# Kernel optimization log

Measured on AMD Instinct MI355X. Metric: run time of the kernel, lower is better.

## Reference

```python
import jax, jax.numpy as jnp
import numpy as np

VO, SO, VIN, SM = 16, 100, 16, 100
B, N, K = 2, 8192, 30
EPS = 1e-8

def _split(x, nv):
    v = x[..., :3 * nv].reshape(x.shape[:-1] + (nv, 3))
    s = x[..., 3 * nv:]
    return v, s

def _merge(v, s):
    return jnp.concatenate([v.reshape(v.shape[:-2] + (-1,)), s], axis=-1)

def _vnorm(v):  # [..., nv, 3] -> [..., nv]
    return jnp.sqrt(jnp.sum(v * v, axis=-1) + EPS)

def gvp(x, nv_in, Wh, Wv, Ws, bs, nls=True, nlv=True):
    v, s = _split(x, nv_in)
    vh = jnp.einsum('...ic,ih->...hc', v, Wh)          # vi -> h vector linear
    vn = _vnorm(vh)                                     # rotation-invariant norms
    s_out = jnp.concatenate([s, vn], axis=-1) @ Ws + bs
    if nls:
        s_out = jax.nn.relu(s_out)
    v_out = jnp.einsum('...hc,ho->...oc', vh, Wv)       # h -> vo vector linear
    if nlv:
        v_out = v_out * jax.nn.sigmoid(_vnorm(v_out))[..., None]
    return _merge(v_out, s_out)

def gvp_layernorm(x, nv, g, b):
    v, s = _split(x, nv)
    vn2 = jnp.sum(v * v, axis=-1, keepdims=True)        # [..., nv, 1]
    denom = jnp.sqrt(jnp.mean(vn2, axis=-2, keepdims=True) + EPS)
    v = v / denom
    mu = jnp.mean(s, axis=-1, keepdims=True)
    var = jnp.var(s, axis=-1, keepdims=True)
    s = (s - mu) / jnp.sqrt(var + 1e-5) * g + b
    return _merge(v, s)

def setup_inputs() -> dict:
    key = jax.random.key(0)
    ks = jax.random.split(key, 24)
    def W(i, shape):
        return jax.random.normal(ks[i], shape, dtype=jnp.float32) / np.float32(np.sqrt(shape[0]))
    d = {}
    d['h_V'] = jax.random.normal(ks[0], (B, N, 3 * VO + SO), dtype=jnp.float32)
    d['h_M'] = jax.random.normal(ks[1], (B, N, K, 3 * VIN + SM), dtype=jnp.float32)
    d['mask_V'] = jax.random.randint(ks[2], (B, N), 0, 2, dtype=jnp.int32)
    d['mask_attend'] = jax.random.randint(ks[3], (B, N, K), 0, 2, dtype=jnp.int32)
    # W_EV: GVP(vi=32,si=200,vo=16,so=100,h=32) -> GVP(16,100,16,100) -> GVP(16,100,16,100,no nl)
    d['Wh1'] = W(4, (32, 32)); d['Wv1'] = W(5, (32, 16)); d['Ws1'] = W(6, (232, 100)); d['bs1'] = jnp.zeros((100,), jnp.float32)
    d['Wh2'] = W(7, (16, 16)); d['Wv2'] = W(8, (16, 16)); d['Ws2'] = W(9, (116, 100)); d['bs2'] = jnp.zeros((100,), jnp.float32)
    d['Wh3'] = W(10, (16, 16)); d['Wv3'] = W(11, (16, 16)); d['Ws3'] = W(12, (116, 100)); d['bs3'] = jnp.zeros((100,), jnp.float32)
    # W_dh: GVP(vi=16,si=100,vo=32,so=400,h=32) -> GVP(vi=32,si=400,vo=16,so=100,h=32,no nl)
    d['Wh4'] = W(13, (16, 32)); d['Wv4'] = W(14, (32, 32)); d['Ws4'] = W(15, (132, 400)); d['bs4'] = jnp.zeros((400,), jnp.float32)
    d['Wh5'] = W(16, (32, 32)); d['Wv5'] = W(17, (32, 16)); d['Ws5'] = W(18, (432, 100)); d['bs5'] = jnp.zeros((100,), jnp.float32)
    d['ln0_g'] = jnp.ones((SO,), jnp.float32); d['ln0_b'] = jnp.zeros((SO,), jnp.float32)
    d['ln1_g'] = jnp.ones((SO,), jnp.float32); d['ln1_b'] = jnp.zeros((SO,), jnp.float32)
    return d

def reference(h_V, h_M, mask_V, mask_attend,
              Wh1, Wv1, Ws1, bs1, Wh2, Wv2, Ws2, bs2, Wh3, Wv3, Ws3, bs3,
              Wh4, Wv4, Ws4, bs4, Wh5, Wv5, Ws5, bs5,
              ln0_g, ln0_b, ln1_g, ln1_b):
    # expand node features over neighbor axis and vs_concat with messages
    hVe = jnp.broadcast_to(h_V[:, :, None, :], (B, N, K, h_V.shape[-1]))
    vV, sV = _split(hVe, VO)
    vM, sM = _split(h_M, VIN)
    h_EV = _merge(jnp.concatenate([vV, vM], axis=-2), jnp.concatenate([sV, sM], axis=-1))
    m = gvp(h_EV, VO + VIN, Wh1, Wv1, Ws1, bs1)
    m = gvp(m, VO, Wh2, Wv2, Ws2, bs2)
    m = gvp(m, VO, Wh3, Wv3, Ws3, bs3, nls=False, nlv=False)
    m = mask_attend[..., None].astype(jnp.float32) * m
    dh = jnp.mean(m, axis=2)
    h = gvp_layernorm(h_V + dh, VO, ln0_g, ln0_b)  # dropout rate 0 -> identity
    dh2 = gvp(h, VO, Wh4, Wv4, Ws4, bs4)
    dh2 = gvp(dh2, 2 * VO, Wh5, Wv5, Ws5, bs5, nls=False, nlv=False)
    h = gvp_layernorm(h + dh2, VO, ln1_g, ln1_b)
    h = mask_V[..., None].astype(jnp.float32) * h
    return h
```

## Files before the change

kernel.cpp:

```cpp
#include <hip/hip_runtime.h>

#define KK 30
#define F 148
#define NNODE 16384

typedef short bf16x8 __attribute__((ext_vector_type(8)));
typedef float f32x4v __attribute__((ext_vector_type(4)));

__device__ __forceinline__ ushort f2bf(float x) {
  unsigned u = __float_as_uint(x);
  unsigned r = (u + 0x7FFF + ((u >> 16) & 1)) >> 16;
  return (ushort)r;
}
__device__ __forceinline__ float bf2f(ushort b) { return __uint_as_float(((unsigned)b) << 16); }
__device__ __forceinline__ void bsplit(float x, ushort& h, ushort& l) {
  ushort hh = f2bf(x); h = hh; l = f2bf(x - bf2f(hh));
}

#define WS_S1B 0
#define WS_VHB (NNODE * 100)
#define WS_WSB (NNODE * 100 + NNODE * 96)
#define B1HI 0
#define B1LO 17920
#define B2HI 35840
#define B2LO 50176
#define B3HI 64512
#define B3LO 78848

__global__ void prep_weights(const float* __restrict__ Ws1, const float* __restrict__ Ws2,
                             const float* __restrict__ Ws3, ushort* __restrict__ ws) {
  int i = blockIdx.x * 256 + threadIdx.x;
  if (i < 17920) {
    int n = i / 160, k = i % 160;
    float w = (n < 100 && k < 132) ? Ws1[(100 + k) * 100 + n] : 0.f;
    ushort h, l; bsplit(w, h, l);
    ws[B1HI + i] = h; ws[B1LO + i] = l;
  } else if (i < 17920 + 14336) {
    int j = i - 17920; int n = j / 128, k = j % 128;
    float w = (n < 100 && k < 116) ? Ws2[k * 100 + n] : 0.f;
    ushort h, l; bsplit(w, h, l);
    ws[B2HI + j] = h; ws[B2LO + j] = l;
  } else if (i < 17920 + 2 * 14336) {
    int j = i - 17920 - 14336; int n = j / 128, k = j % 128;
    float w = (n < 100 && k < 116) ? Ws3[k * 100 + n] : 0.f;
    ushort h, l; bsplit(w, h, l);
    ws[B3HI + j] = h; ws[B3LO + j] = l;
  }
}

__global__ __launch_bounds__(192)
void prep_node(const float* __restrict__ h_V, const float* __restrict__ Ws1,
               const float* __restrict__ bs1, const float* __restrict__ Wh1,
               float* __restrict__ s1bg, float* __restrict__ vhbg) {
  __shared__ float sv[148];
  const int node = blockIdx.x, tid = threadIdx.x;
  for (int f = tid; f < F; f += 192) sv[f] = h_V[(long)node * F + f];
  __syncthreads();
  if (tid < 100) {
    float acc = bs1[tid];
#pragma unroll 4
    for (int i = 0; i < 100; i++) acc = fmaf(sv[48 + i], Ws1[i * 100 + tid], acc);
    s1bg[node * 100 + tid] = acc;
  } else if (tid < 132) {
    int h = tid - 100;
    float a0 = 0.f, a1 = 0.f, a2 = 0.f;
#pragma unroll 4
    for (int i = 0; i < 16; i++) {
      float w = Wh1[i * 32 + h];
      a0 = fmaf(sv[3*i], w, a0); a1 = fmaf(sv[3*i+1], w, a1); a2 = fmaf(sv[3*i+2], w, a2);
    }
    vhbg[node * 96 + 3*h + 0] = a0;
    vhbg[node * 96 + 3*h + 1] = a1;
    vhbg[node * 96 + 3*h + 2] = a2;
  }
}

#define DECL12 float a00=0,a01=0,a02=0,a10=0,a11=0,a12=0,a20=0,a21=0,a22=0,a30=0,a31=0,a32=0;
#define FMA3x4(v0_,v1_,v2_,w_) \
  a00=fmaf(v0_,w_.x,a00); a01=fmaf(v1_,w_.x,a01); a02=fmaf(v2_,w_.x,a02); \
  a10=fmaf(v0_,w_.y,a10); a11=fmaf(v1_,w_.y,a11); a12=fmaf(v2_,w_.y,a12); \
  a20=fmaf(v0_,w_.z,a20); a21=fmaf(v1_,w_.z,a21); a22=fmaf(v2_,w_.z,a22); \
  a30=fmaf(v0_,w_.w,a30); a31=fmaf(v1_,w_.w,a31); a32=fmaf(v2_,w_.w,a32);

#define GATE3(x0,x1,x2,d0,d1,d2) { float vn_=sqrtf((x0)*(x0)+(x1)*(x1)+(x2)*(x2)+1e-8f); \
  float g_=1.f/(1.f+expf(-vn_)); d0=(x0)*g_; d1=(x1)*g_; d2=(x2)*g_; }

template<int NI, bool GATEF>
__device__ __forceinline__ void vtask(const float* vsrc, const float* wbase, int wstride, float* vdst)
{
  DECL12
#pragma unroll 4
  for (int h = 0; h < NI; h++) {
    float v0 = vsrc[3*h], v1 = vsrc[3*h+1], v2 = vsrc[3*h+2];
    float4 w = *(const float4*)(wbase + h * wstride);
    FMA3x4(v0, v1, v2, w)
  }
  if (GATEF) {
    GATE3(a00,a01,a02, vdst[0],vdst[1],vdst[2])
    GATE3(a10,a11,a12, vdst[3],vdst[4],vdst[5])
    GATE3(a20,a21,a22, vdst[6],vdst[7],vdst[8])
    GATE3(a30,a31,a32, vdst[9],vdst[10],vdst[11])
  } else {
    vdst[0]=a00; vdst[1]=a01; vdst[2]=a02;  vdst[3]=a10; vdst[4]=a11; vdst[5]=a12;
    vdst[6]=a20; vdst[7]=a21; vdst[8]=a22;  vdst[9]=a30; vdst[10]=a31; vdst[11]=a32;
  }
}

template<int NI>
__device__ __forceinline__ void vhtaskb(const float* vsrc, const float* wbase, int wstride,
                                        float* vdst, ushort* ncol)
{
  DECL12
#pragma unroll 4
  for (int h = 0; h < NI; h++) {
    float v0 = vsrc[3*h], v1 = vsrc[3*h+1], v2 = vsrc[3*h+2];
    float4 w = *(const float4*)(wbase + h * wstride);
    FMA3x4(v0, v1, v2, w)
  }
  vdst[0]=a00; vdst[1]=a01; vdst[2]=a02;  vdst[3]=a10; vdst[4]=a11; vdst[5]=a12;
  vdst[6]=a20; vdst[7]=a21; vdst[8]=a22;  vdst[9]=a30; vdst[10]=a31; vdst[11]=a32;
  float n0 = sqrtf(a00*a00+a01*a01+a02*a02 + 1e-8f);
  float n1 = sqrtf(a10*a10+a11*a11+a12*a12 + 1e-8f);
  float n2 = sqrtf(a20*a20+a21*a21+a22*a22 + 1e-8f);
  float n3 = sqrtf(a30*a30+a31*a31+a32*a32 + 1e-8f);
  unsigned* p = (unsigned*)ncol;
  p[0] = (unsigned)f2bf(n0) | ((unsigned)f2bf(n1) << 16);
  p[1] = (unsigned)f2bf(n2) | ((unsigned)f2bf(n3) << 16);
}

template<int NKS>
__device__ __forceinline__ void mfma_nt2(const ushort* __restrict__ A, int astr,
                                         const ushort* __restrict__ B_hi,
                                         const ushort* __restrict__ B_lo,
                                         int lane, f32x4v& c0, f32x4v& c1)
{
  int r = lane & 15, q = lane >> 4;
  const int ka = q * 8;
#pragma unroll
  for (int ks = 0; ks < NKS; ks++) {
    int ko = ka + ks * 32;
    bf16x8 a0 = *(const bf16x8*)(A + r * astr + ko);
    bf16x8 a1 = *(const bf16x8*)(A + (16 + r) * astr + ko);
    bf16x8 bh = *(const bf16x8*)(B_hi + ko);
    bf16x8 bl = *(const bf16x8*)(B_lo + ko);
    c0 = __builtin_amdgcn_mfma_f32_16x16x32_bf16(a0, bh, c0, 0, 0, 0);
    c0 = __builtin_amdgcn_mfma_f32_16x16x32_bf16(a0, bl, c0, 0, 0, 0);
    c1 = __builtin_amdgcn_mfma_f32_16x16x32_bf16(a1, bh, c1, 0, 0, 0);
    c1 = __builtin_amdgcn_mfma_f32_16x16x32_bf16(a1, bl, c1, 0, 0, 0);
  }
}

#define P_SV   0
#define P_VA   148
#define P_VB   1618
#define P_MKB  4528
#define P_A    4532
#define P_A2   7220
#define A1S 168
#define A2S 136
#define POOL_F 10220

__global__ __launch_bounds__(256, 4)
void mpnn_fused(const float* __restrict__ h_V, const float* __restrict__ h_M,
                const int* __restrict__ mask_V, const int* __restrict__ mask_attend,
                const float* __restrict__ Wh1, const float* __restrict__ Wv1,
                const float* __restrict__ Wv2, const float* __restrict__ bs2,
                const float* __restrict__ Wv3, const float* __restrict__ bs3,
                const float* __restrict__ Wh2, const float* __restrict__ Wh3,
                const float* __restrict__ Wh4, const float* __restrict__ Wv4,
                const float* __restrict__ Ws4, const float* __restrict__ bs4,
                const float* __restrict__ Wh5, const float* __restrict__ Wv5,
                const float* __restrict__ Ws5, const float* __restrict__ bs5,
                const float* __restrict__ ln0_g, const float* __restrict__ ln0_b,
                const float* __restrict__ ln1_g, const float* __restrict__ ln1_b,
                const float* __restrict__ s1bg, const float* __restrict__ vhbg,
                const ushort* __restrict__ wsb,
                float* __restrict__ out)
{
  __shared__ float pool[POOL_F];
  float* sv   = pool + P_SV;
  float* VAp  = pool + P_VA;
  float* VBp  = pool + P_VB;
  float* sBm  = pool + P_A2;
  ushort* A1 = (ushort*)(pool + P_A);
  ushort* A2 = (ushort*)(pool + P_A2);

  const int tid = threadIdx.x;
  const int node = blockIdx.x;
  const int wave = tid >> 6, lane = tid & 63;

  for (int f = tid; f < F; f += 256) sv[f] = h_V[(long)node * F + f];
  {
    unsigned long long bal = __ballot(tid < KK && mask_attend[node * KK + tid] != 0);
    if (tid == 0) *(unsigned*)(pool + P_MKB) = (unsigned)bal;
  }
  for (int t = tid; t < 448; t += 256) {
    int r = t / 14, c2 = t % 14;
    ((unsigned*)A1)[((r * A1S + 132) >> 1) + c2] = 0;
  }
  for (int t = tid; t < 192; t += 256) {
    int r = t / 6, c2 = t % 6;
    ((unsigned*)A2)[((r * A2S + 116) >> 1) + c2] = 0;
  }
  for (int task = tid; task < KK * 37; task += 256) {
    int k = task / 37, q = task % 37;
    float4 d = *(const float4*)(h_M + ((long)node * KK + k) * F + q * 4);
    if (q < 12) {
      VAp[k * 49 + q * 4 + 0] = d.x; VAp[k * 49 + q * 4 + 1] = d.y;
      VAp[k * 49 + q * 4 + 2] = d.z; VAp[k * 49 + q * 4 + 3] = d.w;
    } else {
      int j0 = q * 4 - 48;
      unsigned* p = (unsigned*)(A1 + k * A1S + j0);
      p[0] = (unsigned)f2bf(d.x) | ((unsigned)f2bf(d.y) << 16);
      p[1] = (unsigned)f2bf(d.z) | ((unsigned)f2bf(d.w) << 16);
    }
  }
  __syncthreads();

  if (tid < 240) {
    int k = tid >> 3, h0 = (tid & 7) * 4;
    const float4* vb4 = (const float4*)(vhbg + (long)node * 96 + 3 * h0);
    float4 q0 = vb4[0], q1 = vb4[1], q2 = vb4[2];
    float a00=q0.x,a01=q0.y,a02=q0.z, a10=q0.w,a11=q1.x,a12=q1.y,
          a20=q1.z,a21=q1.w,a22=q2.x, a30=q2.y,a31=q2.z,a32=q2.w;
#pragma unroll 4
    for (int i = 0; i < 16; i++) {
      float v0 = VAp[k*49+3*i], v1 = VAp[k*49+3*i+1], v2 = VAp[k*49+3*i+2];
      float4 w = *(const float4*)(Wh1 + (16 + i) * 32 + h0);
      FMA3x4(v0, v1, v2, w)
    }
    float* vb = VBp + k * 97 + 3 * h0;
    vb[0]=a00; vb[1]=a01; vb[2]=a02;  vb[3]=a10; vb[4]=a11; vb[5]=a12;
    vb[6]=a20; vb[7]=a21; vb[8]=a22;  vb[9]=a30; vb[10]=a31; vb[11]=a32;
    float n0 = sqrtf(a00*a00+a01*a01+a02*a02 + 1e-8f);
    float n1 = sqrtf(a10*a10+a11*a11+a12*a12 + 1e-8f);
    float n2 = sqrtf(a20*a20+a21*a21+a22*a22 + 1e-8f);
    float n3 = sqrtf(a30*a30+a31*a31+a32*a32 + 1e-8f);
    unsigned* p = (unsigned*)(A1 + k * A1S + 100 + h0);
    p[0] = (unsigned)f2bf(n0) | ((unsigned)f2bf(n1) << 16);
    p[1] = (unsigned)f2bf(n2) | ((unsigned)f2bf(n3) << 16);
  }
  __syncthreads();

  if (wave < 2) {
    int r = lane & 15, q = lane >> 4;
    int nt0 = (wave == 0) ? 0 : 4, nt1 = (wave == 0) ? 4 : 7;
    for (int nt = nt0; nt < nt1; nt++) {
      int n = nt * 16 + r;
      float base = (n < 100) ? s1bg[(long)node * 100 + n] : 0.f;
      f32x4v c0 = {0,0,0,0}, c1 = {0,0,0,0};
      mfma_nt2<5>(A1, A1S, wsb + B1HI + n * 160, wsb + B1LO + n * 160, lane, c0, c1);
      unsigned* dst = (unsigned*)A2;
#pragma unroll
      for (int reg = 0; reg < 4; reg++) {
        int m0 = q * 4 + reg, m1 = m0 + 16;
        unsigned hx = f2bf(fmaxf(c0[reg] + base, 0.f));
        unsigned ox = __shfl_down(hx, 1);
        unsigned hy = f2bf(fmaxf(c1[reg] + base, 0.f));
        unsigned oy = __shfl_down(hy, 1);
        if (((lane & 1) == 0) && n < 100) {
          dst[(m0 * A2S + n) >> 1] = hx | (ox << 16);
          if (m1 < 30) dst[(m1 * A2S + n) >> 1] = hy | (oy << 16);
        }
      }
    }
  } else {
    int vt = tid - 128;
    if (vt < 120) { int k = vt >> 2, o0 = (vt & 3) * 4;
      vtask<32, true>(VBp + k*97, Wv1 + o0, 16, VAp + k*49 + 3*o0); }
  }
  __syncthreads();

  if (tid < 120) {
    int k = tid >> 2, h0 = (tid & 3) * 4;
    vhtaskb<16>(VAp + k*49, Wh2 + h0, 16, VBp + k*97 + 3*h0, A2 + k*A2S + 100 + h0);
  }
  __syncthreads();

  if (wave < 2) {
    int r = lane & 15, q = lane >> 4;
    int nt0 = (wave == 0) ? 0 : 4, nt1 = (wave == 0) ? 4 : 7;
    for (int nt = nt0; nt < nt1; nt++) {
      f32x4v c0 = {0,0,0,0}, c1 = {0,0,0,0};
      int n = nt * 16 + r;
      mfma_nt2<4>(A2, A2S, wsb + B2HI + n * 128, wsb + B2LO + n * 128, lane, c0, c1);
      float base = (n < 100) ? bs2[n] : 0.f;
      unsigned* dst = (unsigned*)A1;
#pragma unroll
      for (int reg = 0; reg < 4; reg++) {
        int m0 = q * 4 + reg, m1 = m0 + 16;
        unsigned hx = f2bf(fmaxf(c0[reg] + base, 0.f));
        unsigned ox = __shfl_down(hx, 1);
        unsigned hy = f2bf(fmaxf(c1[reg] + base, 0.f));
        unsigned oy = __shfl_down(hy, 1);
        if (((lane & 1) == 0) && n < 100) {
          dst[(m0 * A1S + n) >> 1] = hx | (ox << 16);
          if (m1 < 30) dst[(m1 * A1S + n) >> 1] = hy | (oy << 16);
        }
      }
    }
  } else {
    int vt = tid - 128;
    if (vt < 120) { int k = vt >> 2, o0 = (vt & 3) * 4;
      vtask<16, true>(VBp + k*97, Wv2 + o0, 16, VAp + k*49 + 3*o0); }
  }
  __syncthreads();

  if (tid < 120) {
    int k = tid >> 2, h0 = (tid & 3) * 4;
    vhtaskb<16>(VAp + k*49, Wh3 + h0, 16, VBp + k*97 + 3*h0, A1 + k*A1S + 100 + h0);
  } else if (tid >= 240) {
    for (int t = tid - 240; t < 192; t += 16) {
      int r = t / 6, c2 = t % 6;
      ((unsigned*)A1)[((r * A1S + 116) >> 1) + c2] = 0;
    }
  }
  __syncthreads();

  if (wave < 2) {
    int r = lane & 15, q = lane >> 4;
    int nt0 = (wave == 0) ? 0 : 4, nt1 = (wave == 0) ? 4 : 7;
    for (int nt = nt0; nt < nt1; nt++) {
      f32x4v c0 = {0,0,0,0}, c1 = {0,0,0,0};
      int n = nt * 16 + r;
      mfma_nt2<4>(A1, A1S, wsb + B3HI + n * 128, wsb + B3LO + n * 128, lane, c0, c1);
      if (n < 100) {
        float base = bs3[n];
#pragma unroll
        for (int reg = 0; reg < 4; reg++) {
          int m0 = q * 4 + reg, m1 = m0 + 16;
          sBm[m0 * 100 + n] = c0[reg] + base;
          if (m1 < 30) sBm[m1 * 100 + n] = c1[reg] + base;
        }
      }
    }
  } else {
    int vt = tid - 128;
    if (vt < 120) { int k = vt >> 2, o0 = (vt & 3) * 4;
      vtask<16, false>(VBp + k*97, Wv3 + o0, 16, VAp + k*49 + 3*o0); }
  }
  __syncthreads();

  float* ns   = pool + P_A;
  float* xb   = ns;
  float* hb   = ns + 160;
  float* nvh4 = ns + 320;
  float* nvn4 = ns + 416;
  float* s4   = ns + 448;
  float* nvn5 = ns + 848;
  float* v4   = ns + 880;
  float* nvh5 = ns + 976;
  float* v5   = ns + 1072;
  float* s5   = ns + 1120;
  float* red  = ns + 1220;
  float* part = ns + 1232;

  {
    unsigned mkb = *(unsigned*)(pool + P_MKB);
    for (int f = tid; f < F; f += 256) {
      float acc = 0.f;
      if (f < 48) { for (int k = 0; k < KK; k++) if ((mkb >> k) & 1) acc += VAp[k*49 + f]; }
      else        { int j = f - 48; for (int k = 0; k < KK; k++) if ((mkb >> k) & 1) acc += sBm[k*100 + j]; }
      xb[f] = sv[f] + acc * (1.f / (float)KK);
    }
  }
  __syncthreads();
  if (tid < 64) {
    float a = (tid < 50) ? xb[48 + 2 * tid] : 0.f;
    float b = (tid < 50) ? xb[48 + 2 * tid + 1] : 0.f;
    float s = a + b, qq = a * a + b * b;
    for (int off = 32; off; off >>= 1) { s += __shfl_down(s, off); qq += __shfl_down(qq, off); }
    if (tid == 0) { red[1] = s * 0.01f; red[2] = qq * 0.01f; }
  } else if (tid < 128) {
    int l = tid - 64;
    float v = (l < 48) ? xb[l] : 0.f;
    float qq = v * v;
    for (int off = 32; off; off >>= 1) qq += __shfl_down(qq, off);
    if (l == 0) red[0] = sqrtf(qq * (1.f / 16.f) + 1e-8f);
  }
  __syncthreads();
  {
    float denom = red[0], mu = red[1];
    float var = red[2] - mu * mu;
    float rs = rsqrtf(var + 1e-5f);
    for (int f = tid; f < F; f += 256) {
      if (f < 48) hb[f] = xb[f] / denom;
      else { int j = f - 48; hb[f] = (xb[f] - mu) * rs * ln0_g[j] + ln0_b[j]; }
    }
  }
  __syncthreads();

  if (tid < 32) {
    int h = tid;
    float a0 = 0.f, a1 = 0.f, a2 = 0.f;
#pragma unroll 4
    for (int i = 0; i < 16; i++) {
      float w = Wh4[i * 32 + h];
      a0 = fmaf(hb[3*i], w, a0); a1 = fmaf(hb[3*i+1], w, a1); a2 = fmaf(hb[3*i+2], w, a2);
    }
    nvh4[3*h] = a0; nvh4[3*h+1] = a1; nvh4[3*h+2] = a2;
    nvn4[h] = sqrtf(a0*a0 + a1*a1 + a2*a2 + 1e-8f);
  }
  __syncthreads();
  if (tid < 200) {
    int j0 = tid * 2;
    float ax = bs4[j0], ay = bs4[j0 + 1];
    const float* w = Ws4 + j0;
#pragma unroll 4
    for (int i = 0; i < 100; i++) {
      float s = hb[48 + i];
      float2 w2 = *(const float2*)(w + i * 400);
      ax = fmaf(s, w2.x, ax); ay = fmaf(s, w2.y, ay);
    }
#pragma unroll 4
    for (int h = 0; h < 32; h++) {
      float s = nvn4[h];
      float2 w2 = *(const float2*)(w + (100 + h) * 400);
      ax = fmaf(s, w2.x, ax); ay = fmaf(s, w2.y, ay);
    }
    s4[j0] = fmaxf(ax, 0.f); s4[j0 + 1] = fmaxf(ay, 0.f);
  } else if (tid >= 224) {
    int o = tid - 224;
    float a0 = 0.f, a1 = 0.f, a2 = 0.f;
#pragma unroll 4
    for (int h = 0; h < 32; h++) {
      float w = Wv4[h * 32 + o];
      a0 = fmaf(nvh4[3*h], w, a0); a1 = fmaf(nvh4[3*h+1], w, a1); a2 = fmaf(nvh4[3*h+2], w, a2);
    }
    GATE3(a0, a1, a2, v4[3*o], v4[3*o+1], v4[3*o+2])
  }
  __syncthreads();
  if (tid < 32) {
    int h = tid;
    float a0 = 0.f, a1 = 0.f, a2 = 0.f;
#pragma unroll 4
    for (int i = 0; i < 32; i++) {
      float w = Wh5[i * 32 + h];
      a0 = fmaf(v4[3*i], w, a0); a1 = fmaf(v4[3*i+1], w, a1); a2 = fmaf(v4[3*i+2], w, a2);
    }
    nvh5[3*h] = a0; nvh5[3*h+1] = a1; nvh5[3*h+2] = a2;
    nvn5[h] = sqrtf(a0*a0 + a1*a1 + a2*a2 + 1e-8f);
  }
  __syncthreads();
  if (tid < 200) {
    int jq = tid / 8, c = tid % 8, j0 = jq * 4;
    int ibeg = c * 54, iend = ibeg + 54;
    float4 acc = make_float4(0.f, 0.f, 0.f, 0.f);
    const float* w = Ws5 + j0;
#pragma unroll 4
    for (int i = ibeg; i < iend; i++) {
      float s = s4[i];
      float4 w4 = *(const float4*)(w + i * 100);
      acc.x = fmaf(s, w4.x, acc.x); acc.y = fmaf(s, w4.y, acc.y);
      acc.z = fmaf(s, w4.z, acc.z); acc.w = fmaf(s, w4.w, acc.w);
    }
    *(float4*)&part[tid * 4] = acc;
  } else if (tid >= 224 && tid < 240) {
    int o = tid - 224;
    float a0 = 0.f, a1 = 0.f, a2 = 0.f;
#pragma unroll 4
    for (int h = 0; h < 32; h++) {
      float w = Wv5[h * 16 + o];
      a0 = fmaf(nvh5[3*h], w, a0); a1 = fmaf(nvh5[3*h+1], w, a1); a2 = fmaf(nvh5[3*h+2], w, a2);
    }
    v5[3*o] = a0; v5[3*o+1] = a1; v5[3*o+2] = a2;
  }
  __syncthreads();
  if (tid < 25) {
    int j0 = tid * 4;
    float4 b = *(const float4*)(bs5 + j0);
    float4 acc = b;
#pragma unroll
    for (int c = 0; c < 8; c++) {
      float4 p = *(const float4*)&part[(tid * 8 + c) * 4];
      acc.x += p.x; acc.y += p.y; acc.z += p.z; acc.w += p.w;
    }
    *(float4*)&s5[j0] = acc;
  }
  __syncthreads();
  for (int f = tid; f < F; f += 256) {
    float d = (f < 48) ? v5[f] : s5[f - 48];
    xb[f] = hb[f] + d;
  }
  __syncthreads();
  if (tid < 64) {
    float a = (tid < 50) ? xb[48 + 2 * tid] : 0.f;
    float b = (tid < 50) ? xb[48 + 2 * tid + 1] : 0.f;
    float s = a + b, qq = a * a + b * b;
    for (int off = 32; off; off >>= 1) { s += __shfl_down(s, off); qq += __shfl_down(qq, off); }
    if (tid == 0) { red[1] = s * 0.01f; red[2] = qq * 0.01f; }
  } else if (tid < 128) {
    int l = tid - 64;
    float v = (l < 48) ? xb[l] : 0.f;
    float qq = v * v;
    for (int off = 32; off; off >>= 1) qq += __shfl_down(qq, off);
    if (l == 0) red[0] = sqrtf(qq * (1.f / 16.f) + 1e-8f);
  }
  __syncthreads();
  {
    float denom = red[0], mu = red[1];
    float var = red[2] - mu * mu;
    float rs = rsqrtf(var + 1e-5f);
    float mv = (float)mask_V[node];
    for (int f = tid; f < F; f += 256) {
      float val;
      if (f < 48) val = xb[f] / denom;
      else { int j = f - 48; val = (xb[f] - mu) * rs * ln1_g[j] + ln1_b[j]; }
      out[(long)node * F + f] = mv * val;
    }
  }
}

extern "C" void kernel_launch(void* const* d_in, const int* in_sizes, int n_in,
                              void* d_out, int out_size, void* d_ws, size_t ws_size,
                              hipStream_t stream) {
  const float* h_V  = (const float*)d_in[0];
  const float* h_M  = (const float*)d_in[1];
  const int* mask_V = (const int*)d_in[2];
  const int* mask_attend = (const int*)d_in[3];
  const float* Wh1 = (const float*)d_in[4];
  const float* Wv1 = (const float*)d_in[5];
  const float* Ws1 = (const float*)d_in[6];
  const float* bs1 = (const float*)d_in[7];
  const float* Wh2 = (const float*)d_in[8];
  const float* Wv2 = (const float*)d_in[9];
  const float* Ws2 = (const float*)d_in[10];
  const float* bs2 = (const float*)d_in[11];
  const float* Wh3 = (const float*)d_in[12];
  const float* Wv3 = (const float*)d_in[13];
  const float* Ws3 = (const float*)d_in[14];
  const float* bs3 = (const float*)d_in[15];
  const float* Wh4 = (const float*)d_in[16];
  const float* Wv4 = (const float*)d_in[17];
  const float* Ws4 = (const float*)d_in[18];
  const float* bs4 = (const float*)d_in[19];
  const float* Wh5 = (const float*)d_in[20];
  const float* Wv5 = (const float*)d_in[21];
  const float* Ws5 = (const float*)d_in[22];
  const float* bs5 = (const float*)d_in[23];
  const float* ln0_g = (const float*)d_in[24];
  const float* ln0_b = (const float*)d_in[25];
  const float* ln1_g = (const float*)d_in[26];
  const float* ln1_b = (const float*)d_in[27];
  float* out = (float*)d_out;

  float* wsf = (float*)d_ws;
  float* s1bg = wsf + WS_S1B;
  float* vhbg = wsf + WS_VHB;
  ushort* wsb = (ushort*)(wsf + WS_WSB);

  prep_weights<<<dim3(182), dim3(256), 0, stream>>>(Ws1, Ws2, Ws3, wsb);
  prep_node<<<dim3(NNODE), dim3(192), 0, stream>>>(h_V, Ws1, bs1, Wh1, s1bg, vhbg);
  mpnn_fused<<<dim3(NNODE), dim3(256), 0, stream>>>(
      h_V, h_M, mask_V, mask_attend,
      Wh1, Wv1, Wv2, bs2, Wv3, bs3, Wh2, Wh3,
      Wh4, Wv4, Ws4, bs4, Wh5, Wv5, Ws5, bs5,
      ln0_g, ln0_b, ln1_g, ln1_b, s1bg, vhbg, wsb, out);
}
```

Measured before the change: 1.388 ms.

## Store intermediate vectors as bf16 and reduce masked scalar messages in registers

Intermediate vector features in shared memory are now packed as bf16 pairs instead of fp32. The final scalar GVP output is reduced over neighbors directly from MFMA accumulators, using the attend mask and cross-lane shuffles, rather than being written to a shared 30x100 buffer and summed later. The bias is added once, scaled by the mask count. Together this cuts shared memory enough to raise launch bounds from 4 to 5 blocks per CU, at the cost of lower precision for intermediate vectors.

```diff
diff --git a/kernel.cpp b/kernel.cpp
--- a/kernel.cpp
+++ b/kernel.cpp
@@ -13,6 +13,9 @@
   return (ushort)r;
 }
 __device__ __forceinline__ float bf2f(ushort b) { return __uint_as_float(((unsigned)b) << 16); }
+__device__ __forceinline__ unsigned pk2(float x, float y) {
+  return (unsigned)f2bf(x) | ((unsigned)f2bf(y) << 16);
+}
 __device__ __forceinline__ void bsplit(float x, ushort& h, ushort& l) {
   ushort hh = f2bf(x); h = hh; l = f2bf(x - bf2f(hh));
 }
@@ -86,14 +89,20 @@
   float g_=1.f/(1.f+expf(-vn_)); d0=(x0)*g_; d1=(x1)*g_; d2=(x2)*g_; }
 
 template<int NI, bool GATEF>
-__device__ __forceinline__ void vtask(const float* vsrc, const float* wbase, int wstride, float* vdst)
+__device__ __forceinline__ void vtaskb(const unsigned* __restrict__ vsrc,
+                                       const float* __restrict__ wbase, int wstride,
+                                       float* __restrict__ vdst)
 {
   DECL12
 #pragma unroll 4
-  for (int h = 0; h < NI; h++) {
-    float v0 = vsrc[3*h], v1 = vsrc[3*h+1], v2 = vsrc[3*h+2];
-    float4 w = *(const float4*)(wbase + h * wstride);
-    FMA3x4(v0, v1, v2, w)
+  for (int h2 = 0; h2 < NI / 2; h2++) {
+    unsigned d0 = vsrc[3*h2+0], d1 = vsrc[3*h2+1], d2 = vsrc[3*h2+2];
+    float4 w0 = *(const float4*)(wbase + (2*h2) * wstride);
+    float4 w1 = *(const float4*)(wbase + (2*h2+1) * wstride);
+    float e0 = bf2f((ushort)d0), e1 = bf2f((ushort)(d0 >> 16)), e2 = bf2f((ushort)d1);
+    float g0 = bf2f((ushort)(d1 >> 16)), g1 = bf2f((ushort)d2), g2 = bf2f((ushort)(d2 >> 16));
+    FMA3x4(e0, e1, e2, w0)
+    FMA3x4(g0, g1, g2, w1)
   }
   if (GATEF) {
     GATE3(a00,a01,a02, vdst[0],vdst[1],vdst[2])
@@ -107,8 +116,9 @@
 }
 
 template<int NI>
-__device__ __forceinline__ void vhtaskb(const float* vsrc, const float* wbase, int wstride,
-                                        float* vdst, ushort* ncol)
+__device__ __forceinline__ void vhtaskb(const float* __restrict__ vsrc,
+                                        const float* __restrict__ wbase, int wstride,
+                                        unsigned* __restrict__ vdst_u, ushort* __restrict__ ncol)
 {
   DECL12
 #pragma unroll 4
@@ -117,15 +127,14 @@
     float4 w = *(const float4*)(wbase + h * wstride);
     FMA3x4(v0, v1, v2, w)
   }
-  vdst[0]=a00; vdst[1]=a01; vdst[2]=a02;  vdst[3]=a10; vdst[4]=a11; vdst[5]=a12;
-  vdst[6]=a20; vdst[7]=a21; vdst[8]=a22;  vdst[9]=a30; vdst[10]=a31; vdst[11]=a32;
+  vdst_u[0] = pk2(a00,a01); vdst_u[1] = pk2(a02,a10); vdst_u[2] = pk2(a11,a12);
+  vdst_u[3] = pk2(a20,a21); vdst_u[4] = pk2(a22,a30); vdst_u[5] = pk2(a31,a32);
   float n0 = sqrtf(a00*a00+a01*a01+a02*a02 + 1e-8f);
   float n1 = sqrtf(a10*a10+a11*a11+a12*a12 + 1e-8f);
   float n2 = sqrtf(a20*a20+a21*a21+a22*a22 + 1e-8f);
   float n3 = sqrtf(a30*a30+a31*a31+a32*a32 + 1e-8f);
   unsigned* p = (unsigned*)ncol;
-  p[0] = (unsigned)f2bf(n0) | ((unsigned)f2bf(n1) << 16);
-  p[1] = (unsigned)f2bf(n2) | ((unsigned)f2bf(n3) << 16);
+  p[0] = pk2(n0, n1); p[1] = pk2(n2, n3);
 }
 
 template<int NKS>
@@ -151,16 +160,17 @@
 }
 
 #define P_SV   0
-#define P_VA   148
-#define P_VB   1618
-#define P_MKB  4528
-#define P_A    4532
-#define P_A2   7220
-#define A1S 168
+#define P_MKB  148
+#define P_VA   152
+#define P_VB   1624
+#define P_DH   3064
+#define P_A2   3164
+#define P_A    5340
+#define A1S 160
 #define A2S 136
-#define POOL_F 10220
-
-__global__ __launch_bounds__(256, 4)
+#define POOL_F 7900
+
+__global__ __launch_bounds__(256, 5)
 void mpnn_fused(const float* __restrict__ h_V, const float* __restrict__ h_M,
                 const int* __restrict__ mask_V, const int* __restrict__ mask_attend,
                 const float* __restrict__ Wh1, const float* __restrict__ Wv1,
@@ -180,8 +190,8 @@
   __shared__ float pool[POOL_F];
   float* sv   = pool + P_SV;
   float* VAp  = pool + P_VA;
-  float* VBp  = pool + P_VB;
-  float* sBm  = pool + P_A2;
+  ushort* VBu = (ushort*)(pool + P_VB);
+  float* dhs  = pool + P_DH;
   ushort* A1 = (ushort*)(pool + P_A);
   ushort* A2 = (ushort*)(pool + P_A2);
 
@@ -229,16 +239,15 @@
       float4 w = *(const float4*)(Wh1 + (16 + i) * 32 + h0);
       FMA3x4(v0, v1, v2, w)
     }
-    float* vb = VBp + k * 97 + 3 * h0;
-    vb[0]=a00; vb[1]=a01; vb[2]=a02;  vb[3]=a10; vb[4]=a11; vb[5]=a12;
-    vb[6]=a20; vb[7]=a21; vb[8]=a22;  vb[9]=a30; vb[10]=a31; vb[11]=a32;
+    unsigned* vb = (unsigned*)(VBu + k * 96 + 3 * h0);
+    vb[0]=pk2(a00,a01); vb[1]=pk2(a02,a10); vb[2]=pk2(a11,a12);
+    vb[3]=pk2(a20,a21); vb[4]=pk2(a22,a30); vb[5]=pk2(a31,a32);
     float n0 = sqrtf(a00*a00+a01*a01+a02*a02 + 1e-8f);
     float n1 = sqrtf(a10*a10+a11*a11+a12*a12 + 1e-8f);
     float n2 = sqrtf(a20*a20+a21*a21+a22*a22 + 1e-8f);
     float n3 = sqrtf(a30*a30+a31*a31+a32*a32 + 1e-8f);
     unsigned* p = (unsigned*)(A1 + k * A1S + 100 + h0);
-    p[0] = (unsigned)f2bf(n0) | ((unsigned)f2bf(n1) << 16);
-    p[1] = (unsigned)f2bf(n2) | ((unsigned)f2bf(n3) << 16);
+    p[0] = pk2(n0, n1); p[1] = pk2(n2, n3);
   }
   __syncthreads();
 
@@ -267,13 +276,14 @@
   } else {
     int vt = tid - 128;
     if (vt < 120) { int k = vt >> 2, o0 = (vt & 3) * 4;
-      vtask<32, true>(VBp + k*97, Wv1 + o0, 16, VAp + k*49 + 3*o0); }
+      vtaskb<32, true>((const unsigned*)(VBu + k * 96), Wv1 + o0, 16, VAp + k*49 + 3*o0); }
   }
   __syncthreads();
 
   if (tid < 120) {
     int k = tid >> 2, h0 = (tid & 3) * 4;
-    vhtaskb<16>(VAp + k*49, Wh2 + h0, 16, VBp + k*97 + 3*h0, A2 + k*A2S + 100 + h0);
+    vhtaskb<16>(VAp + k*49, Wh2 + h0, 16,
+                (unsigned*)(VBu + k*96 + 3*h0), A2 + k*A2S + 100 + h0);
   }
   __syncthreads();
 
@@ -302,13 +312,14 @@
   } else {
     int vt = tid - 128;
     if (vt < 120) { int k = vt >> 2, o0 = (vt & 3) * 4;
-      vtask<16, true>(VBp + k*97, Wv2 + o0, 16, VAp + k*49 + 3*o0); }
+      vtaskb<16, true>((const unsigned*)(VBu + k * 96), Wv2 + o0, 16, VAp + k*49 + 3*o0); }
   }
   __syncthreads();
 
   if (tid < 120) {
     int k = tid >> 2, h0 = (tid & 3) * 4;
-    vhtaskb<16>(VAp + k*49, Wh3 + h0, 16, VBp + k*97 + 3*h0, A1 + k*A1S + 100 + h0);
+    vhtaskb<16>(VAp + k*49, Wh3 + h0, 16,
+                (unsigned*)(VBu + k*96 + 3*h0), A1 + k*A1S + 100 + h0);
   } else if (tid >= 240) {
     for (int t = tid - 240; t < 192; t += 16) {
       int r = t / 6, c2 = t % 6;
@@ -318,26 +329,28 @@
   __syncthreads();
 
   if (wave < 2) {
+    unsigned mkb = *(unsigned*)(pool + P_MKB);
     int r = lane & 15, q = lane >> 4;
     int nt0 = (wave == 0) ? 0 : 4, nt1 = (wave == 0) ? 4 : 7;
     for (int nt = nt0; nt < nt1; nt++) {
       f32x4v c0 = {0,0,0,0}, c1 = {0,0,0,0};
       int n = nt * 16 + r;
       mfma_nt2<4>(A1, A1S, wsb + B3HI + n * 128, wsb + B3LO + n * 128, lane, c0, c1);
-      if (n < 100) {
-        float base = bs3[n];
+      float part = 0.f;
 #pragma unroll
-        for (int reg = 0; reg < 4; reg++) {
-          int m0 = q * 4 + reg, m1 = m0 + 16;
-          sBm[m0 * 100 + n] = c0[reg] + base;
-          if (m1 < 30) sBm[m1 * 100 + n] = c1[reg] + base;
-        }
+      for (int reg = 0; reg < 4; reg++) {
+        int m0 = q * 4 + reg, m1 = m0 + 16;
+        part += ((mkb >> m0) & 1) ? c0[reg] : 0.f;
+        part += ((mkb >> m1) & 1) ? c1[reg] : 0.f;
       }
+      part += __shfl_xor(part, 16);
+      part += __shfl_xor(part, 32);
+      if (q == 0 && n < 100) dhs[n] = part;
     }
   } else {
     int vt = tid - 128;
     if (vt < 120) { int k = vt >> 2, o0 = (vt & 3) * 4;
-      vtask<16, false>(VBp + k*97, Wv3 + o0, 16, VAp + k*49 + 3*o0); }
+      vtaskb<16, false>((const unsigned*)(VBu + k * 96), Wv3 + o0, 16, VAp + k*49 + 3*o0); }
   }
   __syncthreads();
 
@@ -357,10 +370,11 @@
 
   {
     unsigned mkb = *(unsigned*)(pool + P_MKB);
+    float cntf = (float)__popc(mkb);
     for (int f = tid; f < F; f += 256) {
-      float acc = 0.f;
-      if (f < 48) { for (int k = 0; k < KK; k++) if ((mkb >> k) & 1) acc += VAp[k*49 + f]; }
-      else        { int j = f - 48; for (int k = 0; k < KK; k++) if ((mkb >> k) & 1) acc += sBm[k*100 + j]; }
+      float acc;
+      if (f < 48) { acc = 0.f; for (int k = 0; k < KK; k++) if ((mkb >> k) & 1) acc += VAp[k*49 + f]; }
+      else        { int j = f - 48; acc = dhs[j] + cntf * bs3[j]; }
       xb[f] = sv[f] + acc * (1.f / (float)KK);
     }
   }
```

Result: faster. 1.334 ms (-3.9%).
